# Kernel optimization log

Measured on AMD Instinct MI355X. Metric: run time of the kernel, lower is better.

Reference implementation:

```python
import jax, jax.numpy as jnp
import numpy as np

N = 50000          # n_nodes
E_RAND = 800000    # random edges (before self-loops)
D_FEAT = 128
ALPHA = 0.1
NITER = 10


def setup_inputs() -> dict:
    key = jax.random.key(0)
    k1, k2, k3 = jax.random.split(key, 3)
    r = jax.random.randint(k1, (E_RAND,), 0, N)
    c = jax.random.randint(k2, (E_RAND,), 0, N)
    loop = jnp.arange(N)
    # A + I  (self-loops appended, matching calc_A_hat's sp.eye addition)
    rows = jnp.concatenate([r, loop]).astype(jnp.int32)   # [850000]
    cols = jnp.concatenate([c, loop]).astype(jnp.int32)   # [850000]
    # D_vec = row sums of (A + I); symmetric normalization D^-1/2 (A+I) D^-1/2
    deg = jax.ops.segment_sum(jnp.ones(rows.shape[0], jnp.float32), rows, num_segments=N)
    dinv = 1.0 / jnp.sqrt(jnp.maximum(deg, 1.0))
    # A_hat values pre-scaled by (1 - alpha), as registered in the buffer
    vals = ((1.0 - ALPHA) * dinv[rows] * dinv[cols]).astype(jnp.float32)
    E = jax.random.normal(k3, (N, D_FEAT), dtype=jnp.float32)
    return {"E": E, "rows": rows, "cols": cols, "vals": vals}


def reference(E, rows, cols, vals):
    # preds_{t+1} = A_hat @ preds_t + alpha * E   (niter power-iteration steps)
    # spmm via gather + segment_sum over the COO edge list.
    def step(preds, _):
        msg = vals[:, None] * preds[cols]                       # [nnz, d]
        preds = jax.ops.segment_sum(msg, rows, num_segments=N) + ALPHA * E
        return preds, None
    out, _ = jax.lax.scan(step, E, None, length=NITER)
    return out
```

## Files before the change

kernel.cpp:

```cpp
#include <hip/hip_runtime.h>


#define ALPHA 0.1f
#define NITER 10
#define DFEAT 128
#define CHUNK 1024


__global__ void zero_ints(int* __restrict__ p, int n) {
    int i = blockIdx.x * blockDim.x + threadIdx.x;
    if (i < n) p[i] = 0;
}

__global__ void hist_rows(const int* __restrict__ rows, int* __restrict__ counts, int nnz) {
    int e = blockIdx.x * blockDim.x + threadIdx.x;
    if (e < nnz) atomicAdd(&counts[rows[e]], 1);
}

__global__ void scan_reduce(const int* __restrict__ counts, int* __restrict__ blockSums, int N) {
    __shared__ int lds[256];
    int b = blockIdx.x, t = threadIdx.x;
    int base = b * CHUNK + t * 4;
    int s = 0;
    if (base + 4 <= N) {
        int4 v = *(const int4*)(counts + base);
        s = v.x + v.y + v.z + v.w;
    } else {
        for (int k = 0; k < 4; ++k) if (base + k < N) s += counts[base + k];
    }
    lds[t] = s;
    __syncthreads();
    for (int off = 128; off > 0; off >>= 1) {
        if (t < off) lds[t] += lds[t + off];
        __syncthreads();
    }
    if (t == 0) blockSums[b] = lds[0];
}

__global__ void scan_blocksums(const int* __restrict__ blockSums, int* __restrict__ blockOff,
                               int* __restrict__ rowptr, int NB, int N) {
    __shared__ int lds[1024];
    int t = threadIdx.x;
    int v = (t < NB) ? blockSums[t] : 0;
    lds[t] = v;
    __syncthreads();
    for (int off = 1; off < 1024; off <<= 1) {
        int u = (t >= off) ? lds[t - off] : 0;
        __syncthreads();
        lds[t] += u;
        __syncthreads();
    }
    if (t < NB) blockOff[t] = (t == 0) ? 0 : lds[t - 1];
    if (t == 1023) rowptr[N] = lds[1023];
}

__global__ void scan_write(const int* __restrict__ counts, const int* __restrict__ blockOff,
                           int* __restrict__ rowptr, int N) {
    __shared__ int lds[256];
    int b = blockIdx.x, t = threadIdx.x;
    int base = b * CHUNK + t * 4;
    int c0 = 0, c1 = 0, c2 = 0, c3 = 0;
    if (base + 4 <= N) {
        int4 v = *(const int4*)(counts + base);
        c0 = v.x; c1 = v.y; c2 = v.z; c3 = v.w;
    } else {
        if (base + 0 < N) c0 = counts[base + 0];
        if (base + 1 < N) c1 = counts[base + 1];
        if (base + 2 < N) c2 = counts[base + 2];
        if (base + 3 < N) c3 = counts[base + 3];
    }
    int s = c0 + c1 + c2 + c3;
    lds[t] = s;
    __syncthreads();
    for (int off = 1; off < 256; off <<= 1) {
        int u = (t >= off) ? lds[t - off] : 0;
        __syncthreads();
        lds[t] += u;
        __syncthreads();
    }
    int run = ((t == 0) ? 0 : lds[t - 1]) + blockOff[b];
    if (base + 0 < N) { rowptr[base + 0] = run; run += c0; }
    if (base + 1 < N) { rowptr[base + 1] = run; run += c1; }
    if (base + 2 < N) { rowptr[base + 2] = run; run += c2; }
    if (base + 3 < N) { rowptr[base + 3] = run; run += c3; }
}

__global__ void copy_ints(const int* __restrict__ src, int* __restrict__ dst, int n) {
    int i = blockIdx.x * blockDim.x + threadIdx.x;
    if (i < n) dst[i] = src[i];
}

__global__ void build_csr(const int* __restrict__ rows, const int* __restrict__ cols,
                          const float* __restrict__ vals, int* __restrict__ offsets,
                          int2* __restrict__ packed, int nnz) {
    int e = blockIdx.x * blockDim.x + threadIdx.x;
    if (e >= nnz) return;
    int r = rows[e];
    int pos = atomicAdd(&offsets[r], 1);
    int2 p;
    p.x = cols[e] << 8;
    p.y = __float_as_int(vals[e]);
    packed[pos] = p;
}


__device__ inline unsigned f32_to_bf16_rne(float f) {
    unsigned x = __float_as_uint(f);
    return (x + 0x7fffu + ((x >> 16) & 1u)) >> 16;
}

#define GATH(k)                                                                 \
    int2 p##k = packed[i + k];                                                  \
    unsigned u##k = 0; float2 x##k = {0.f, 0.f};                                \
    if constexpr (SRCB) {                                                       \
        u##k = *(const unsigned*)(sp + (size_t)(unsigned)p##k.x + loff);        \
    } else {                                                                    \
        x##k = *(const float2*)(sp + ((size_t)(unsigned)p##k.x << 1) + loff);   \
    }

#define ACC(k)                                                                  \
    {   float v = __int_as_float(p##k.y);                                       \
        if constexpr (SRCB) {                                                   \
            x##k.x = __uint_as_float(u##k << 16);                               \
            x##k.y = __uint_as_float(u##k & 0xffff0000u);                       \
        }                                                                       \
        acc.x += v * x##k.x;                                                    \
        acc.y += v * x##k.y; }

template <bool SRCB, bool DSTB>
__global__ void spmm_t(const int* __restrict__ rowptr, const int2* __restrict__ packed,
                       const void* __restrict__ src, const float* __restrict__ E,
                       void* __restrict__ dst, int N) {
    int gw   = (blockIdx.x * blockDim.x + threadIdx.x) >> 6;
    int nw   = (gridDim.x * blockDim.x) >> 6;
    int lane = threadIdx.x & 63;
    const size_t loff = (size_t)lane * (SRCB ? 4 : 8);
    const char* sp = (const char*)src;

    for (int w = gw; w < N; w += nw) {
        int s = rowptr[w];
        int e = rowptr[w + 1];

        float2 ev = ((const float2*)(E + (size_t)w * DFEAT))[lane];
        float2 acc = {ALPHA * ev.x, ALPHA * ev.y};

        int i = s;
        for (; i + 16 <= e; i += 16) {
            GATH(0) GATH(1) GATH(2) GATH(3) GATH(4) GATH(5) GATH(6) GATH(7)
            GATH(8) GATH(9) GATH(10) GATH(11) GATH(12) GATH(13) GATH(14) GATH(15)
            ACC(0) ACC(1) ACC(2) ACC(3) ACC(4) ACC(5) ACC(6) ACC(7)
            ACC(8) ACC(9) ACC(10) ACC(11) ACC(12) ACC(13) ACC(14) ACC(15)
        }
        for (; i + 8 <= e; i += 8) {
            GATH(0) GATH(1) GATH(2) GATH(3) GATH(4) GATH(5) GATH(6) GATH(7)
            ACC(0) ACC(1) ACC(2) ACC(3) ACC(4) ACC(5) ACC(6) ACC(7)
        }
        for (; i + 4 <= e; i += 4) {
            GATH(0) GATH(1) GATH(2) GATH(3)
            ACC(0) ACC(1) ACC(2) ACC(3)
        }
        for (; i < e; ++i) {
            GATH(0)
            ACC(0)
        }

        if constexpr (DSTB) {
            unsigned wbits = f32_to_bf16_rne(acc.x) | (f32_to_bf16_rne(acc.y) << 16);
            *(unsigned*)((char*)dst + (size_t)w * 256 + (size_t)lane * 4) = wbits;
        } else {
            ((float2*)((float*)dst + (size_t)w * DFEAT))[lane] = acc;
        }
    }
}

#undef GATH
#undef ACC

extern "C" void kernel_launch(void* const* d_in, const int* in_sizes, int n_in,
                              void* d_out, int out_size, void* d_ws, size_t ws_size,
                              hipStream_t stream) {
    const float* E    = (const float*)d_in[0];
    const int*   rows = (const int*)d_in[1];
    const int*   cols = (const int*)d_in[2];
    const float* vals = (const float*)d_in[3];
    float*       out  = (float*)d_out;

    const int nd  = in_sizes[0];
    const int nnz = in_sizes[1];
    const int N   = nd / DFEAT;
    const int NB  = (N + CHUNK - 1) / CHUNK;

    const int Np  = (N + 4 + 3) & ~3;
    const int NBp = (NB + 3) & ~3;
    char* ws = (char*)d_ws;
    char*  bufA    = ws;
    char*  bufB    = ws + (size_t)nd * 2;
    int*   rowptr  = (int*)(ws + (size_t)nd * 4);
    int*   offs    = rowptr + Np;
    int*   bsums   = offs + Np;
    int*   boff    = bsums + NBp;
    int2*  packed  = (int2*)((char*)(boff + NBp));

    dim3 blk(256);
    dim3 gN((N + 255) / 256);
    dim3 gE((nnz + 255) / 256);

    zero_ints<<<gN, blk, 0, stream>>>(offs, N);
    hist_rows<<<gE, blk, 0, stream>>>(rows, offs, nnz);
    scan_reduce<<<NB, 256, 0, stream>>>(offs, bsums, N);
    scan_blocksums<<<1, 1024, 0, stream>>>(bsums, boff, rowptr, NB, N);
    scan_write<<<NB, 256, 0, stream>>>(offs, boff, rowptr, N);
    copy_ints<<<gN, blk, 0, stream>>>(rowptr, offs, N);
    build_csr<<<gE, blk, 0, stream>>>(rows, cols, vals, offs, packed, nnz);

    dim3 gS(2048);
    spmm_t<false, true><<<gS, blk, 0, stream>>>(rowptr, packed, E, E, bufA, N);
    char* cur = bufA;
    char* nxt = bufB;
    for (int it = 2; it <= NITER - 1; ++it) {
        spmm_t<true, true><<<gS, blk, 0, stream>>>(rowptr, packed, cur, E, nxt, N);
        char* t = cur; cur = nxt; nxt = t;
    }
    spmm_t<true, false><<<gS, blk, 0, stream>>>(rowptr, packed, cur, E, out, N);
}
```

Measured before the change: 487.3 us.

## Split SpMM into two feature-half passes over a bf16 source

Each SpMM iteration now runs as two launches, each covering 64 of the 128 features, so every gathered source working set is half as large (25 KB-ish rows become 128 B segments) and may fit better in cache. The input E is first converted to bf16 so every iteration, including the first, reads bf16. Setup is also trimmed: the zero kernel becomes a memset and the offsets copy is folded into scan_write. The cost is reading the CSR index/value stream twice per iteration and using 2-byte per-lane gathers, which give narrower memory transactions.

```diff
diff --git a/kernel.cpp b/kernel.cpp
--- a/kernel.cpp
+++ b/kernel.cpp
@@ -4,13 +4,9 @@
 #define ALPHA 0.1f
 #define NITER 10
 #define DFEAT 128
+#define HALF  64
 #define CHUNK 1024
 
-
-__global__ void zero_ints(int* __restrict__ p, int n) {
-    int i = blockIdx.x * blockDim.x + threadIdx.x;
-    if (i < n) p[i] = 0;
-}
 
 __global__ void hist_rows(const int* __restrict__ rows, int* __restrict__ counts, int nnz) {
     int e = blockIdx.x * blockDim.x + threadIdx.x;
@@ -55,7 +51,7 @@
 }
 
 __global__ void scan_write(const int* __restrict__ counts, const int* __restrict__ blockOff,
-                           int* __restrict__ rowptr, int N) {
+                           int* __restrict__ rowptr, int* __restrict__ offs, int N) {
     __shared__ int lds[256];
     int b = blockIdx.x, t = threadIdx.x;
     int base = b * CHUNK + t * 4;
@@ -79,15 +75,10 @@
         __syncthreads();
     }
     int run = ((t == 0) ? 0 : lds[t - 1]) + blockOff[b];
-    if (base + 0 < N) { rowptr[base + 0] = run; run += c0; }
-    if (base + 1 < N) { rowptr[base + 1] = run; run += c1; }
-    if (base + 2 < N) { rowptr[base + 2] = run; run += c2; }
-    if (base + 3 < N) { rowptr[base + 3] = run; run += c3; }
-}
-
-__global__ void copy_ints(const int* __restrict__ src, int* __restrict__ dst, int n) {
-    int i = blockIdx.x * blockDim.x + threadIdx.x;
-    if (i < n) dst[i] = src[i];
+    if (base + 0 < N) { rowptr[base + 0] = run; offs[base + 0] = run; run += c0; }
+    if (base + 1 < N) { rowptr[base + 1] = run; offs[base + 1] = run; run += c1; }
+    if (base + 2 < N) { rowptr[base + 2] = run; offs[base + 2] = run; run += c2; }
+    if (base + 3 < N) { rowptr[base + 3] = run; offs[base + 3] = run; run += c3; }
 }
 
 __global__ void build_csr(const int* __restrict__ rows, const int* __restrict__ cols,
@@ -109,40 +100,39 @@
     return (x + 0x7fffu + ((x >> 16) & 1u)) >> 16;
 }
 
+__global__ void cvt_f32_bf16(const float2* __restrict__ in, unsigned* __restrict__ out, int n2) {
+    int i = blockIdx.x * blockDim.x + threadIdx.x;
+    if (i < n2) {
+        float2 v = in[i];
+        out[i] = f32_to_bf16_rne(v.x) | (f32_to_bf16_rne(v.y) << 16);
+    }
+}
+
+
 #define GATH(k)                                                                 \
     int2 p##k = packed[i + k];                                                  \
-    unsigned u##k = 0; float2 x##k = {0.f, 0.f};                                \
-    if constexpr (SRCB) {                                                       \
-        u##k = *(const unsigned*)(sp + (size_t)(unsigned)p##k.x + loff);        \
-    } else {                                                                    \
-        x##k = *(const float2*)(sp + ((size_t)(unsigned)p##k.x << 1) + loff);   \
-    }
+    unsigned short u##k = *(const unsigned short*)(sp + (size_t)(unsigned)p##k.x + loff);
 
 #define ACC(k)                                                                  \
     {   float v = __int_as_float(p##k.y);                                       \
-        if constexpr (SRCB) {                                                   \
-            x##k.x = __uint_as_float(u##k << 16);                               \
-            x##k.y = __uint_as_float(u##k & 0xffff0000u);                       \
-        }                                                                       \
-        acc.x += v * x##k.x;                                                    \
-        acc.y += v * x##k.y; }
-
-template <bool SRCB, bool DSTB>
-__global__ void spmm_t(const int* __restrict__ rowptr, const int2* __restrict__ packed,
-                       const void* __restrict__ src, const float* __restrict__ E,
-                       void* __restrict__ dst, int N) {
+        float x = __uint_as_float(((unsigned)u##k) << 16);                      \
+        acc += v * x; }
+
+template <bool DSTB>
+__global__ void spmm_half(const int* __restrict__ rowptr, const int2* __restrict__ packed,
+                          const char* __restrict__ srcb, const float* __restrict__ E,
+                          void* __restrict__ dst, int N, int passOff) {
     int gw   = (blockIdx.x * blockDim.x + threadIdx.x) >> 6;
     int nw   = (gridDim.x * blockDim.x) >> 6;
     int lane = threadIdx.x & 63;
-    const size_t loff = (size_t)lane * (SRCB ? 4 : 8);
-    const char* sp = (const char*)src;
+    const size_t loff = ((size_t)passOff + lane) * 2;
+    const char* sp = srcb;
 
     for (int w = gw; w < N; w += nw) {
         int s = rowptr[w];
         int e = rowptr[w + 1];
 
-        float2 ev = ((const float2*)(E + (size_t)w * DFEAT))[lane];
-        float2 acc = {ALPHA * ev.x, ALPHA * ev.y};
+        float acc = ALPHA * E[(size_t)w * DFEAT + passOff + lane];
 
         int i = s;
         for (; i + 16 <= e; i += 16) {
@@ -165,10 +155,10 @@
         }
 
         if constexpr (DSTB) {
-            unsigned wbits = f32_to_bf16_rne(acc.x) | (f32_to_bf16_rne(acc.y) << 16);
-            *(unsigned*)((char*)dst + (size_t)w * 256 + (size_t)lane * 4) = wbits;
+            *(unsigned short*)((char*)dst + (size_t)w * 256 + loff) =
+                (unsigned short)f32_to_bf16_rne(acc);
         } else {
-            ((float2*)((float*)dst + (size_t)w * DFEAT))[lane] = acc;
+            ((float*)dst)[(size_t)w * DFEAT + passOff + lane] = acc;
         }
     }
 }
@@ -202,24 +192,26 @@
     int2*  packed  = (int2*)((char*)(boff + NBp));
 
     dim3 blk(256);
-    dim3 gN((N + 255) / 256);
     dim3 gE((nnz + 255) / 256);
 
-    zero_ints<<<gN, blk, 0, stream>>>(offs, N);
+    hipMemsetAsync(offs, 0, (size_t)N * 4, stream);
     hist_rows<<<gE, blk, 0, stream>>>(rows, offs, nnz);
     scan_reduce<<<NB, 256, 0, stream>>>(offs, bsums, N);
     scan_blocksums<<<1, 1024, 0, stream>>>(bsums, boff, rowptr, NB, N);
-    scan_write<<<NB, 256, 0, stream>>>(offs, boff, rowptr, N);
-    copy_ints<<<gN, blk, 0, stream>>>(rowptr, offs, N);
+    scan_write<<<NB, 256, 0, stream>>>(offs, boff, rowptr, offs, N);
     build_csr<<<gE, blk, 0, stream>>>(rows, cols, vals, offs, packed, nnz);
 
+    const int n2 = nd / 2;
+    cvt_f32_bf16<<<(n2 + 255) / 256, blk, 0, stream>>>((const float2*)E, (unsigned*)bufB, n2);
+
     dim3 gS(2048);
-    spmm_t<false, true><<<gS, blk, 0, stream>>>(rowptr, packed, E, E, bufA, N);
-    char* cur = bufA;
-    char* nxt = bufB;
-    for (int it = 2; it <= NITER - 1; ++it) {
-        spmm_t<true, true><<<gS, blk, 0, stream>>>(rowptr, packed, cur, E, nxt, N);
+    char* cur = bufB;
+    char* nxt = bufA;
+    for (int it = 1; it <= NITER - 1; ++it) {
+        spmm_half<true><<<gS, blk, 0, stream>>>(rowptr, packed, cur, E, nxt, N, 0);
+        spmm_half<true><<<gS, blk, 0, stream>>>(rowptr, packed, cur, E, nxt, N, HALF);
         char* t = cur; cur = nxt; nxt = t;
     }
-    spmm_t<true, false><<<gS, blk, 0, stream>>>(rowptr, packed, cur, E, out, N);
-}
+    spmm_half<false><<<gS, blk, 0, stream>>>(rowptr, packed, cur, E, out, N, 0);
+    spmm_half<false><<<gS, blk, 0, stream>>>(rowptr, packed, cur, E, out, N, HALF);
+}
```

After: 667.8 us. +37.0%, slower.
